# Performance work log

Measured on AMD Instinct MI355X. Metric: run time of the kernel, lower is better.

## Reference

```python
import jax, jax.numpy as jnp
import numpy as np

# Scaled Llama backbone (NF4 dequant-matmul == dense matmul math) + LoRA(q,v) + cls head
L, V, D, H, F, R, C = 4, 32000, 2048, 16, 8192, 16, 3
HD = D // H  # 128, matches real Llama head_dim
ALPHA_OVER_R = 32.0 / R
EPS = 1e-5
NEG = -1e9


def setup_inputs() -> dict:
    B, S = 2, 1024
    keys = iter(jax.random.split(jax.random.key(0), 40))

    def rn(shape, s=0.02):
        return jax.random.normal(next(keys), shape, dtype=jnp.float32) * s

    return {
        "input_ids": jax.random.randint(next(keys), (B, S), 0, V),
        "attention_mask": jnp.ones((B, S), dtype=jnp.int32),
        "embed": rn((V, D)),
        "Wq": rn((L, D, D)), "Wk": rn((L, D, D)), "Wv": rn((L, D, D)), "Wo": rn((L, D, D)),
        "Aq": rn((L, R, D)), "Bq": rn((L, D, R)), "Av": rn((L, R, D)), "Bv": rn((L, D, R)),
        "Wg": rn((L, F, D)), "Wu": rn((L, F, D)), "Wd": rn((L, D, F)),
        "norm1": jnp.ones((L, D)), "norm2": jnp.ones((L, D)), "final_norm": jnp.ones((D,)),
        "head_W1": rn((D, D)), "head_b1": jnp.zeros((D,)),
        "head_W2": rn((C, D)), "head_b2": jnp.zeros((C,)),
    }


def _rms(x, w):
    return x * w * jax.lax.rsqrt(jnp.mean(x * x, -1, keepdims=True) + EPS)


def _rope_tables(S):
    inv = 1.0 / (10000.0 ** (jnp.arange(0, HD, 2, dtype=jnp.float32) / HD))
    f = jnp.outer(jnp.arange(S, dtype=jnp.float32), inv)  # [S, HD//2]
    emb = jnp.concatenate([f, f], -1)                      # [S, HD]
    return jnp.cos(emb), jnp.sin(emb)


def _rot(x):
    return jnp.concatenate([-x[..., HD // 2:], x[..., :HD // 2]], -1)


def reference(input_ids, attention_mask, embed, Wq, Wk, Wv, Wo, Aq, Bq, Av, Bv,
              Wg, Wu, Wd, norm1, norm2, final_norm, head_W1, head_b1, head_W2, head_b2):
    B, S = input_ids.shape
    x = embed[input_ids]                                   # [B,S,D]
    cos, sin = _rope_tables(S)
    causal = jnp.tril(jnp.ones((S, S), dtype=bool))
    mask = jnp.where(causal[None, None], 0.0, NEG) \
        + (1.0 - attention_mask.astype(jnp.float32))[:, None, None, :] * NEG  # [B,1,S,S]

    for l in range(L):  # small fixed layer count
        h = _rms(x, norm1[l])

        def proj(W):
            return jnp.einsum('bsd,ed->bse', h, W)

        def lora(A, Bm):
            return ALPHA_OVER_R * jnp.einsum('bsr,er->bse', jnp.einsum('bsd,rd->bsr', h, A), Bm)

        q = (proj(Wq[l]) + lora(Aq[l], Bq[l])).reshape(B, S, H, HD)
        k = proj(Wk[l]).reshape(B, S, H, HD)
        v = (proj(Wv[l]) + lora(Av[l], Bv[l])).reshape(B, S, H, HD)
        q = q * cos[None, :, None, :] + _rot(q) * sin[None, :, None, :]
        k = k * cos[None, :, None, :] + _rot(k) * sin[None, :, None, :]

        scores = jnp.einsum('bqhd,bkhd->bhqk', q, k) / np.float32(np.sqrt(HD)) + mask
        attn = jax.nn.softmax(scores, -1)
        o = jnp.einsum('bhqk,bkhd->bqhd', attn, v).reshape(B, S, D)
        x = x + jnp.einsum('bsd,ed->bse', o, Wo[l])

        h2 = _rms(x, norm2[l])
        g = jnp.einsum('bsd,fd->bsf', h2, Wg[l])
        u = jnp.einsum('bsd,fd->bsf', h2, Wu[l])
        x = x + jnp.einsum('bsf,df->bsd', jax.nn.silu(g) * u, Wd[l])

    x = _rms(x, final_norm)
    # LlamaForSequenceClassification pooling at last non-pad token; score = Identity
    idx = jnp.sum(attention_mask, -1) - 1
    pooled = x[jnp.arange(B), idx].astype(jnp.float32)     # [B, D]
    # head_layer (dropout = identity in eval)
    h = jnp.tanh(pooled @ head_W1.T + head_b1)
    return h @ head_W2.T + head_b2                          # [B, C]
```

## Files before the change

kernel.cpp:

```cpp
#include <hip/hip_runtime.h>

#define NLAYER 4
#define DMODEL 2048
#define NHEAD  16
#define HEADD  128
#define FFDIM  8192
#define RLORA  16
#define SEQLEN 1024
#define NBATCH 2
#define NTOK   (NBATCH*SEQLEN)
#define QKVS   6144

typedef __bf16 bf16x8 __attribute__((ext_vector_type(8)));
typedef float  f32x4  __attribute__((ext_vector_type(4)));
typedef unsigned short us8 __attribute__((ext_vector_type(8)));

__device__ __forceinline__ unsigned short f2b(float f) {
  unsigned int u = __builtin_bit_cast(unsigned int, f);
  u += 0x7FFFu + ((u >> 16) & 1u);
  return (unsigned short)(u >> 16);
}
__device__ __forceinline__ float b2f(unsigned short s) {
  unsigned int u = ((unsigned int)s) << 16;
  return __builtin_bit_cast(float, u);
}
__device__ __forceinline__ int vswz(int d) {
  return (((d >> 2) & 7) ^ ((d & 3) << 1)) << 4;
}
typedef __attribute__((address_space(1))) const void* gas_t;
typedef __attribute__((address_space(3))) void* las_t;
__device__ __forceinline__ void gload16(const void* g, void* l) {
  __builtin_amdgcn_global_load_lds((gas_t)g, (las_t)l, 16, 0, 0);
}

__global__ void k_embed(const int* __restrict__ ids, const float* __restrict__ emb,
                        float* __restrict__ x) {
  int row = blockIdx.x;
  int id = ids[row];
  const float4* src = (const float4*)(emb + (size_t)id * DMODEL);
  float4* dst = (float4*)(x + (size_t)row * DMODEL);
  for (int i = threadIdx.x; i < DMODEL / 4; i += 256) dst[i] = src[i];
}

__global__ void k_cvt16(const float* __restrict__ s, unsigned short* __restrict__ d, int n8) {
  int stride = gridDim.x * 256;
  for (int i = blockIdx.x * 256 + threadIdx.x; i < n8; i += stride) {
    size_t si = (size_t)i * 2;
    float4 a = ((const float4*)s)[si];
    float4 b = ((const float4*)s)[si + 1];
    us8 o;
    o[0]=f2b(a.x); o[1]=f2b(a.y); o[2]=f2b(a.z); o[3]=f2b(a.w);
    o[4]=f2b(b.x); o[5]=f2b(b.y); o[6]=f2b(b.z); o[7]=f2b(b.w);
    ((us8*)d)[i] = o;
  }
}

__global__ void k_cvtqkv(const float* __restrict__ Wq, const float* __restrict__ Wk,
                         const float* __restrict__ Wv, unsigned short* __restrict__ d) {
  const size_t DD8 = (size_t)DMODEL * DMODEL / 8;
  const int n8 = (int)(NLAYER * 3 * DD8);
  int stride = gridDim.x * 256;
  for (int i = blockIdx.x * 256 + threadIdx.x; i < n8; i += stride) {
    int lay = i / (int)(3 * DD8);
    int rem = i - lay * (int)(3 * DD8);
    int ten = rem / (int)DD8;
    int off = rem - ten * (int)DD8;
    const float* s = (ten == 0 ? Wq : ten == 1 ? Wk : Wv) + (size_t)lay * DMODEL * DMODEL;
    float4 a = ((const float4*)s)[(size_t)off * 2];
    float4 b = ((const float4*)s)[(size_t)off * 2 + 1];
    us8 o;
    o[0]=f2b(a.x); o[1]=f2b(a.y); o[2]=f2b(a.z); o[3]=f2b(a.w);
    o[4]=f2b(b.x); o[5]=f2b(b.y); o[6]=f2b(b.z); o[7]=f2b(b.w);
    ((us8*)(d))[(size_t)i] = o;
  }
}

__global__ void k_rmsnorm(const float* __restrict__ x, const float* __restrict__ w,
                          unsigned short* __restrict__ h) {
  int row = blockIdx.x, t = threadIdx.x;
  const float* xr = x + (size_t)row * DMODEL;
  float4 a = ((const float4*)xr)[t];
  float4 b = ((const float4*)xr)[t + 256];
  float ss = a.x*a.x + a.y*a.y + a.z*a.z + a.w*a.w
           + b.x*b.x + b.y*b.y + b.z*b.z + b.w*b.w;
  for (int m = 32; m; m >>= 1) ss += __shfl_xor(ss, m);
  __shared__ float red[4];
  if ((t & 63) == 0) red[t >> 6] = ss;
  __syncthreads();
  ss = red[0] + red[1] + red[2] + red[3];
  float rs = rsqrtf(ss * (1.0f / DMODEL) + 1e-5f);
  float4 wa = ((const float4*)w)[t];
  float4 wb = ((const float4*)w)[t + 256];
  ushort4 oa, ob;
  oa.x = f2b(a.x * wa.x * rs); oa.y = f2b(a.y * wa.y * rs);
  oa.z = f2b(a.z * wa.z * rs); oa.w = f2b(a.w * wa.w * rs);
  ob.x = f2b(b.x * wb.x * rs); ob.y = f2b(b.y * wb.y * rs);
  ob.z = f2b(b.z * wb.z * rs); ob.w = f2b(b.w * wb.w * rs);
  ushort4* hr = (ushort4*)(h + (size_t)row * DMODEL);
  hr[t] = oa;
  hr[t + 256] = ob;
}

template<int MODE>
__global__ __launch_bounds__(512, 4)
void k_gemm5(const unsigned short* __restrict__ A, const unsigned short* __restrict__ B,
             float* __restrict__ Cf, unsigned short* __restrict__ Cb,
             const float* __restrict__ Res, const unsigned short* __restrict__ Gaux,
             int N, int K, int ldc) {
  __shared__ unsigned short As[8192];
  __shared__ unsigned short Bs[16384];
  const int t = threadIdx.x, l = t & 63, w = t >> 6;
  const int wm = w >> 2, wn = w & 3;
  const int nbx = gridDim.x;
  const int nwg = nbx * gridDim.y;
  const int bid = blockIdx.y * nbx + blockIdx.x;
  const int sid = (bid & 7) * (nwg >> 3) + (bid >> 3);
  const int m0 = (sid / nbx) << 7;
  const int n0 = (sid % nbx) << 8;
  const int srow = (w << 3) + (l >> 3);
  const int gcol = 8 * ((l & 7) ^ ((srow >> 1) & 7));
  const unsigned short* Ag = A + (size_t)(m0 + srow) * K + gcol;
  const unsigned short* Bg = B + (size_t)(n0 + srow) * K + gcol;
  const size_t r64K = (size_t)64 * K;
  unsigned short* AsW = As + (w << 9);
  unsigned short* BsW = Bs + (w << 9);
  const int cl = l & 15, lh = l >> 4;
  const int fR = (cl >> 1) & 7;
  f32x4 acc[4][4];
  #pragma unroll
  for (int mi = 0; mi < 4; mi++)
    #pragma unroll
    for (int ni = 0; ni < 4; ni++) { f32x4 z = {0.f,0.f,0.f,0.f}; acc[mi][ni] = z; }

  for (int kt = 0; kt < K; kt += 64) {
    gload16(Ag + kt,          AsW);
    gload16(Ag + kt +   r64K, AsW + 4096);
    gload16(Bg + kt,          BsW);
    gload16(Bg + kt +   r64K, BsW + 4096);
    gload16(Bg + kt + 2*r64K, BsW + 8192);
    gload16(Bg + kt + 3*r64K, BsW + 12288);
    __syncthreads();
    #pragma unroll
    for (int kh = 0; kh < 2; kh++) {
      const int so = ((kh * 4 + lh) ^ fR) << 4;
      bf16x8 af[4], bf[4];
      #pragma unroll
      for (int i = 0; i < 4; i++) {
        af[i] = *(const bf16x8*)((const char*)As + (wm*64 + i*16 + cl) * 128 + so);
        bf[i] = *(const bf16x8*)((const char*)Bs + (wn*64 + i*16 + cl) * 128 + so);
      }
      #pragma unroll
      for (int mi = 0; mi < 4; mi++)
        #pragma unroll
        for (int ni = 0; ni < 4; ni++)
          acc[mi][ni] = __builtin_amdgcn_mfma_f32_16x16x32_bf16(af[mi], bf[ni], acc[mi][ni], 0, 0, 0);
    }
    __syncthreads();
  }
  const int rbase = lh << 2;
  #pragma unroll
  for (int mi = 0; mi < 4; mi++) {
    #pragma unroll
    for (int ni = 0; ni < 4; ni++) {
      #pragma unroll
      for (int rr = 0; rr < 4; rr++) {
        int row = m0 + wm * 64 + mi * 16 + rbase + rr;
        int col = n0 + wn * 64 + ni * 16 + cl;
        size_t idx = (size_t)row * ldc + col;
        float val = acc[mi][ni][rr];
        if constexpr (MODE == 0) Cf[idx] = val;
        if constexpr (MODE == 1) Cf[idx] = val + Res[idx];
        if constexpr (MODE == 2) Cb[idx] = f2b(val);
        if constexpr (MODE == 3) {
          float gv = b2f(Gaux[idx]);
          val *= gv / (1.0f + __expf(-gv));
          Cb[idx] = f2b(val);
        }
      }
    }
  }
}

template<int MODE>
__global__ __launch_bounds__(256, 4)
void k_gemm6(const unsigned short* __restrict__ A, const unsigned short* __restrict__ B,
             float* __restrict__ Cf, unsigned short* __restrict__ Cb,
             const float* __restrict__ Res, const unsigned short* __restrict__ Gaux,
             int N, int K, int ldc) {
  __shared__ unsigned short As[4096];
  __shared__ unsigned short Bs[8192];
  const int t = threadIdx.x, l = t & 63, w = t >> 6;
  const int nbx = gridDim.x;
  const int nwg = nbx * gridDim.y;
  const int bid = blockIdx.y * nbx + blockIdx.x;
  const int sid = (bid & 7) * (nwg >> 3) + (bid >> 3);
  const int m0 = (sid / nbx) << 6;
  const int n0 = (sid % nbx) << 7;
  const int srow = (w << 3) + (l >> 3);
  const int gcol = 8 * ((l & 7) ^ ((srow >> 1) & 7));
  const unsigned short* Ag = A + (size_t)(m0 + srow) * K + gcol;
  const unsigned short* Bg = B + (size_t)(n0 + srow) * K + gcol;
  const size_t r32K = (size_t)32 * K;
  unsigned short* AsW = As + (w << 9);
  unsigned short* BsW = Bs + (w << 9);
  const int cl = l & 15, lh = l >> 4;
  const int fR = (cl >> 1) & 7;
  f32x4 acc[4][2];
  #pragma unroll
  for (int mi = 0; mi < 4; mi++)
    #pragma unroll
    for (int ni = 0; ni < 2; ni++) { f32x4 z = {0.f,0.f,0.f,0.f}; acc[mi][ni] = z; }

  for (int kt = 0; kt < K; kt += 64) {
    gload16(Ag + kt,          AsW);
    gload16(Ag + kt +   r32K, AsW + 2048);
    gload16(Bg + kt,          BsW);
    gload16(Bg + kt +   r32K, BsW + 2048);
    gload16(Bg + kt + 2*r32K, BsW + 4096);
    gload16(Bg + kt + 3*r32K, BsW + 6144);
    __syncthreads();
    #pragma unroll
    for (int kh = 0; kh < 2; kh++) {
      const int so = ((kh * 4 + lh) ^ fR) << 4;
      bf16x8 af[4], bf[2];
      #pragma unroll
      for (int mi = 0; mi < 4; mi++)
        af[mi] = *(const bf16x8*)((const char*)As + (mi*16 + cl) * 128 + so);
      #pragma unroll
      for (int ni = 0; ni < 2; ni++)
        bf[ni] = *(const bf16x8*)((const char*)Bs + (w*32 + ni*16 + cl) * 128 + so);
      #pragma unroll
      for (int mi = 0; mi < 4; mi++)
        #pragma unroll
        for (int ni = 0; ni < 2; ni++)
          acc[mi][ni] = __builtin_amdgcn_mfma_f32_16x16x32_bf16(af[mi], bf[ni], acc[mi][ni], 0, 0, 0);
    }
    __syncthreads();
  }
  const int rbase = lh << 2;
  #pragma unroll
  for (int mi = 0; mi < 4; mi++) {
    #pragma unroll
    for (int ni = 0; ni < 2; ni++) {
      #pragma unroll
      for (int rr = 0; rr < 4; rr++) {
        int row = m0 + mi * 16 + rbase + rr;
        int col = n0 + w * 32 + ni * 16 + cl;
        size_t idx = (size_t)row * ldc + col;
        float val = acc[mi][ni][rr];
        if constexpr (MODE == 0) Cf[idx] = val;
        if constexpr (MODE == 1) Cf[idx] = val + Res[idx];
        if constexpr (MODE == 2) Cb[idx] = f2b(val);
        if constexpr (MODE == 3) {
          float gv = b2f(Gaux[idx]);
          val *= gv / (1.0f + __expf(-gv));
          Cb[idx] = f2b(val);
        }
      }
    }
  }
}

template<int MODE>
__global__ __launch_bounds__(256, 2)
void k_gemm2(const unsigned short* __restrict__ A, const void* __restrict__ Bv,
             float* __restrict__ Cf, unsigned short* __restrict__ Cb,
             const float* __restrict__ Res, const unsigned short* __restrict__ Gaux,
             int N, int K, int ldc,
             const float* __restrict__ ltq, const float* __restrict__ ltv,
             const float* __restrict__ lbq, const float* __restrict__ lbv) {
  __shared__ unsigned short As[16384];
  __shared__ unsigned short Bs[16384];
  const unsigned short* B = (const unsigned short*)Bv;
  const int t = threadIdx.x, l = t & 63, w = t >> 6;
  const int wr = w >> 1, wc = w & 1;
  const int nbx = gridDim.x;
  const int nwg = nbx * gridDim.y;
  const int bid = blockIdx.y * nbx + blockIdx.x;
  const int sid = (bid & 7) * (nwg >> 3) + (bid >> 3);
  const int m0 = (sid / nbx) << 7, n0 = (sid % nbx) << 7;
  const int srow = (w << 3) + (l >> 3);
  const int gcol = 8 * ((l & 7) ^ ((srow >> 1) & 7));
  const unsigned short* Ag = A + (size_t)(m0 + srow) * K + gcol;
  const unsigned short* Bg = B + (size_t)(n0 + srow) * K + gcol;
  const size_t r32K = (size_t)32 * K;
  const int cl = l & 15, lh = l >> 4;
  const int fR = (cl >> 1) & 7;
  const int rowA = wr * 64 + cl;
  const int rowB = wc * 64 + cl;
  f32x4 acc[4][4];
  #pragma unroll
  for (int mi = 0; mi < 4; mi++)
    #pragma unroll
    for (int ni = 0; ni < 4; ni++) { f32x4 z = {0.f,0.f,0.f,0.f}; acc[mi][ni] = z; }

  const int NT = K >> 6;
#define STAGE2(buf, kt) do {                                        \
    const unsigned short* ap_ = Ag + (size_t)(kt) * 64;             \
    const unsigned short* bp_ = Bg + (size_t)(kt) * 64;             \
    unsigned short* al_ = As + (buf) * 8192 + (w << 9);             \
    unsigned short* bl_ = Bs + (buf) * 8192 + (w << 9);             \
    gload16(ap_,            al_);                                   \
    gload16(ap_ +   r32K,   al_ + 2048);                            \
    gload16(ap_ + 2*r32K,   al_ + 4096);                            \
    gload16(ap_ + 3*r32K,   al_ + 6144);                            \
    gload16(bp_,            bl_);                                   \
    gload16(bp_ +   r32K,   bl_ + 2048);                            \
    gload16(bp_ + 2*r32K,   bl_ + 4096);                            \
    gload16(bp_ + 3*r32K,   bl_ + 6144);                            \
  } while (0)

  STAGE2(0, 0);
  for (int kt = 0; kt < NT; kt++) {
    const int cur = kt & 1;
    if (kt + 1 < NT) {
      STAGE2(cur ^ 1, kt + 1);
      __builtin_amdgcn_sched_barrier(0);
      asm volatile("s_waitcnt vmcnt(8)" ::: "memory");
    } else {
      __builtin_amdgcn_sched_barrier(0);
      asm volatile("s_waitcnt vmcnt(0)" ::: "memory");
    }
    __builtin_amdgcn_s_barrier();
    __builtin_amdgcn_sched_barrier(0);
    const char* Ab = (const char*)As + cur * 16384;
    const char* Bb = (const char*)Bs + cur * 16384;
    #pragma unroll
    for (int kh = 0; kh < 2; kh++) {
      const int so = ((kh * 4 + lh) ^ fR) << 4;
      bf16x8 af[4], bf[4];
      #pragma unroll
      for (int i = 0; i < 4; i++) {
        af[i] = *(const bf16x8*)(Ab + (rowA + 16*i) * 128 + so);
        bf[i] = *(const bf16x8*)(Bb + (rowB + 16*i) * 128 + so);
      }
      #pragma unroll
      for (int mi = 0; mi < 4; mi++)
        #pragma unroll
        for (int ni = 0; ni < 4; ni++)
          acc[mi][ni] = __builtin_amdgcn_mfma_f32_16x16x32_bf16(af[mi], bf[ni], acc[mi][ni], 0, 0, 0);
    }
    __builtin_amdgcn_sched_barrier(0);
    __builtin_amdgcn_s_barrier();
  }
#undef STAGE2
  const int rbase = lh << 2;
  if constexpr (MODE == 4) {
    #pragma unroll
    for (int ni = 0; ni < 4; ni++) {
      int col = n0 + wc * 64 + ni * 16 + cl;
      const float* lt = nullptr;
      const float* lb = nullptr;
      if (col < 2048)       { lt = ltq; lb = lbq + (size_t)col * RLORA; }
      else if (col >= 4096) { lt = ltv; lb = lbv + (size_t)(col - 4096) * RLORA; }
      float4 b0 = {0,0,0,0}, b1 = b0, b2 = b0, b3 = b0;
      if (lt) {
        b0 = ((const float4*)lb)[0]; b1 = ((const float4*)lb)[1];
        b2 = ((const float4*)lb)[2]; b3 = ((const float4*)lb)[3];
      }
      #pragma unroll
      for (int mi = 0; mi < 4; mi++) {
        #pragma unroll
        for (int rr = 0; rr < 4; rr++) {
          int row = m0 + wr * 64 + mi * 16 + rbase + rr;
          float val = acc[mi][ni][rr];
          if (lt) {
            const float4* tr = (const float4*)(lt + (size_t)row * RLORA);
            float4 t0 = tr[0], t1 = tr[1], t2 = tr[2], t3 = tr[3];
            float dt = t0.x*b0.x + t0.y*b0.y + t0.z*b0.z + t0.w*b0.w
                     + t1.x*b1.x + t1.y*b1.y + t1.z*b1.z + t1.w*b1.w
                     + t2.x*b2.x + t2.y*b2.y + t2.z*b2.z + t2.w*b2.w
                     + t3.x*b3.x + t3.y*b3.y + t3.z*b3.z + t3.w*b3.w;
            val += 2.0f * dt;
          }
          Cf[(size_t)row * ldc + col] = val;
        }
      }
    }
  } else {
    #pragma unroll
    for (int mi = 0; mi < 4; mi++) {
      #pragma unroll
      for (int ni = 0; ni < 4; ni++) {
        #pragma unroll
        for (int rr = 0; rr < 4; rr++) {
          int row = m0 + wr * 64 + mi * 16 + rbase + rr;
          int col = n0 + wc * 64 + ni * 16 + cl;
          size_t idx = (size_t)row * ldc + col;
          float val = acc[mi][ni][rr];
          if constexpr (MODE == 0) Cf[idx] = val;
          if constexpr (MODE == 1) Cf[idx] = val + Res[idx];
          if constexpr (MODE == 2) Cb[idx] = f2b(val);
          if constexpr (MODE == 3) {
            float gv = b2f(Gaux[idx]);
            val *= gv / (1.0f + __expf(-gv));
            Cb[idx] = f2b(val);
          }
        }
      }
    }
  }
}

template<int MODE>
__global__ __launch_bounds__(256, 2)
void k_gemm(const unsigned short* __restrict__ A, const void* __restrict__ Bv,
            float* __restrict__ Cf, unsigned short* __restrict__ Cb,
            const float* __restrict__ Res, const unsigned short* __restrict__ Gaux,
            int N, int K, int ldc) {
  __shared__ unsigned char lds[128 * 32 * 2 * 2];
  unsigned char* As = lds;
  unsigned char* Bs = lds + 128 * 32 * 2;
  const int t = threadIdx.x;
  const int l = t & 63, w = t >> 6;
  const int wr = w >> 1, wc = w & 1;
  const int m0 = blockIdx.y << 7, n0 = blockIdx.x << 7;
  const int sr = t >> 1, skh = (t & 1) << 4;
  const int sByte = sr * 64 + (skh << 1);
  const int sSwz = (sr & 3) << 4;
  const unsigned short* Ap = A + (size_t)(m0 + sr) * K + skh;
  const float* Bp32 = (const float*)Bv + (size_t)(n0 + sr) * K + skh;
  const int kOff = (((l >> 4) << 4)) ^ ((l & 3) << 4);
  const int arow = wr * 64 + (l & 15);
  const int brow = wc * 64 + (l & 15);
  f32x4 acc[4][4];
  #pragma unroll
  for (int mi = 0; mi < 4; mi++)
    #pragma unroll
    for (int ni = 0; ni < 4; ni++) { f32x4 z = {0.f,0.f,0.f,0.f}; acc[mi][ni] = z; }

  for (int kt = 0; kt < K; kt += 32) {
    uint4 a0 = *(const uint4*)(Ap + kt);
    uint4 a1 = *(const uint4*)(Ap + kt + 8);
    *(uint4*)(As + ((sByte)      ^ sSwz)) = a0;
    *(uint4*)(As + ((sByte + 16) ^ sSwz)) = a1;
    float4 f0 = *(const float4*)(Bp32 + kt);
    float4 f1 = *(const float4*)(Bp32 + kt + 4);
    float4 f2 = *(const float4*)(Bp32 + kt + 8);
    float4 f3 = *(const float4*)(Bp32 + kt + 12);
    us8 q0, q1;
    q0[0]=f2b(f0.x); q0[1]=f2b(f0.y); q0[2]=f2b(f0.z); q0[3]=f2b(f0.w);
    q0[4]=f2b(f1.x); q0[5]=f2b(f1.y); q0[6]=f2b(f1.z); q0[7]=f2b(f1.w);
    q1[0]=f2b(f2.x); q1[1]=f2b(f2.y); q1[2]=f2b(f2.z); q1[3]=f2b(f2.w);
    q1[4]=f2b(f3.x); q1[5]=f2b(f3.y); q1[6]=f2b(f3.z); q1[7]=f2b(f3.w);
    *(us8*)(Bs + ((sByte)      ^ sSwz)) = q0;
    *(us8*)(Bs + ((sByte + 16) ^ sSwz)) = q1;
    __syncthreads();
    bf16x8 af[4], bfr[4];
    #pragma unroll
    for (int i = 0; i < 4; i++) {
      af[i]  = *(const bf16x8*)(As + (arow + 16 * i) * 64 + kOff);
      bfr[i] = *(const bf16x8*)(Bs + (brow + 16 * i) * 64 + kOff);
    }
    #pragma unroll
    for (int mi = 0; mi < 4; mi++)
      #pragma unroll
      for (int ni = 0; ni < 4; ni++)
        acc[mi][ni] = __builtin_amdgcn_mfma_f32_16x16x32_bf16(af[mi], bfr[ni], acc[mi][ni], 0, 0, 0);
    __syncthreads();
  }
  const int rbase = (l >> 4) << 2;
  const int cl = l & 15;
  #pragma unroll
  for (int mi = 0; mi < 4; mi++) {
    #pragma unroll
    for (int ni = 0; ni < 4; ni++) {
      #pragma unroll
      for (int rr = 0; rr < 4; rr++) {
        int row = m0 + wr * 64 + mi * 16 + rbase + rr;
        int col = n0 + wc * 64 + ni * 16 + cl;
        size_t idx = (size_t)row * ldc + col;
        float val = acc[mi][ni][rr];
        if constexpr (MODE == 0) Cf[idx] = val;
        if constexpr (MODE == 1) Cf[idx] = val + Res[idx];
        if constexpr (MODE == 2) Cb[idx] = f2b(val);
        if constexpr (MODE == 3) {
          float gv = b2f(Gaux[idx]);
          val *= gv / (1.0f + __expf(-gv));
          Cb[idx] = f2b(val);
        }
      }
    }
  }
}

__global__ void k_lora_down(const unsigned short* __restrict__ h, const float* __restrict__ Am,
                            float* __restrict__ tb) {
  int t = threadIdx.x;
  int m = blockIdx.x * 16 + (t >> 4), r = t & 15;
  const unsigned short* hr = h + (size_t)m * DMODEL;
  const float* ar = Am + (size_t)r * DMODEL;
  float acc = 0.f;
  for (int d = 0; d < DMODEL; d += 4) {
    ushort4 hv = *(const ushort4*)(hr + d);
    float4 av = *(const float4*)(ar + d);
    acc += b2f(hv.x)*av.x + b2f(hv.y)*av.y + b2f(hv.z)*av.z + b2f(hv.w)*av.w;
  }
  tb[(size_t)m * RLORA + r] = acc;
}

__global__ void k_lora_up(const float* __restrict__ tb, const float* __restrict__ Bm,
                          float* __restrict__ out, int ldc) {
  int tid = blockIdx.x * 256 + threadIdx.x;
  int m = tid >> 11, e = tid & (DMODEL - 1);
  const float* tr = tb + (size_t)m * RLORA;
  const float* br = Bm + (size_t)e * RLORA;
  float acc = 0.f;
  #pragma unroll
  for (int r = 0; r < RLORA; r += 4) {
    float4 tv = *(const float4*)(tr + r);
    float4 bv = *(const float4*)(br + r);
    acc += tv.x*bv.x + tv.y*bv.y + tv.z*bv.z + tv.w*bv.w;
  }
  out[(size_t)m * ldc + e] += 2.0f * acc;
}

__global__ void k_rope_table(float* __restrict__ ct, float* __restrict__ st) {
  int tid = blockIdx.x * 256 + threadIdx.x;
  int s = tid >> 6, i = tid & 63;
  float inv = __expf(-((float)i / 64.0f) * logf(10000.0f));
  float ang = (float)s * inv;
  ct[tid] = cosf(ang);
  st[tid] = sinf(ang);
}

__global__ void k_rope2(const float* __restrict__ qkv,
                        const float* __restrict__ ct, const float* __restrict__ st,
                        unsigned short* __restrict__ qb, unsigned short* __restrict__ kb,
                        unsigned short* __restrict__ vb) {
  int tid = blockIdx.x * 256 + threadIdx.x;
  int i = tid & 63;
  int hh = (tid >> 6) & (NHEAD - 1);
  int s = (tid >> 10) & (SEQLEN - 1);
  int b = tid >> 20;
  size_t ibase = ((size_t)(b * SEQLEN + s)) * QKVS + hh * HEADD;
  size_t obase = ((size_t)(b * SEQLEN + s)) * DMODEL + hh * HEADD;
  float c = ct[s * 64 + i], sn = st[s * 64 + i];
  float q0 = qkv[ibase + i], q1 = qkv[ibase + i + 64];
  qb[obase + i]      = f2b(q0 * c - q1 * sn);
  qb[obase + i + 64] = f2b(q1 * c + q0 * sn);
  float k0 = qkv[ibase + 2048 + i], k1 = qkv[ibase + 2048 + i + 64];
  kb[obase + i]      = f2b(k0 * c - k1 * sn);
  kb[obase + i + 64] = f2b(k1 * c + k0 * sn);
  vb[obase + i]      = f2b(qkv[ibase + 4096 + i]);
  vb[obase + i + 64] = f2b(qkv[ibase + 4096 + i + 64]);
}

__global__ __launch_bounds__(256, 2)
void k_attn_bf16(const unsigned short* __restrict__ qbp, const unsigned short* __restrict__ kbp,
                 const unsigned short* __restrict__ vbp, const int* __restrict__ am,
                 unsigned short* __restrict__ o, int vstride) {
  __shared__ unsigned char Kls[64 * 256];
  __shared__ unsigned char Vls[128 * 128];
  __shared__ unsigned char Pls[64 * 128];
  const int qt = blockIdx.x, hh = blockIdx.y, b = blockIdx.z;
  const int t = threadIdx.x, l = t & 63, w = t >> 6;
  const int cl = l & 15, lh = l >> 4;
  const int rbase = lh << 2;

  for (int ii = 0; ii < 4; ii++) {
    int idx = t + 256 * ii; int row = idx >> 4; int c = idx & 15;
    uint4 u = *(const uint4*)(qbp + ((size_t)(b*SEQLEN + qt*64 + row)) * DMODEL + hh * HEADD + c * 8);
    *(uint4*)(Kls + ((row * 256 + c * 16) ^ ((row & 7) << 4))) = u;
  }
  __syncthreads();
  bf16x8 qf[4];
  {
    int row = w * 16 + cl;
    int swz = (row & 7) << 4;
    #pragma unroll
    for (int kt = 0; kt < 4; kt++)
      qf[kt] = *(const bf16x8*)(Kls + ((row * 256 + kt * 64 + lh * 16) ^ swz));
  }

  f32x4 oacc[8];
  #pragma unroll
  for (int i = 0; i < 8; i++) { f32x4 z = {0.f,0.f,0.f,0.f}; oacc[i] = z; }
  float mrun[4], lrun[4];
  #pragma unroll
  for (int r = 0; r < 4; r++) { mrun[r] = -3e38f; lrun[r] = 0.f; }

  for (int kb = 0; kb <= qt; kb++) {
    __syncthreads();
    for (int ii = 0; ii < 4; ii++) {
      int idx = t + 256 * ii; int row = idx >> 4; int c = idx & 15;
      uint4 u = *(const uint4*)(kbp + ((size_t)(b*SEQLEN + kb*64 + row)) * DMODEL + hh * HEADD + c * 8);
      *(uint4*)(Kls + ((row * 256 + c * 16) ^ ((row & 7) << 4))) = u;
    }
    for (int ii = 0; ii < 4; ii++) {
      int idx = t + 256 * ii;
      int n = idx >> 4, dc = idx & 15;
      uint4 a = *(const uint4*)(vbp + ((size_t)(b*SEQLEN + kb*64 + n)) * vstride + hh * HEADD + dc * 8);
      uint4 p;
      p.x = __shfl_xor(a.x, 16); p.y = __shfl_xor(a.y, 16);
      p.z = __shfl_xor(a.z, 16); p.w = __shfl_xor(a.w, 16);
      if (!(l & 16)) {
        int d0 = dc * 8, nb = n * 2;
        unsigned int wd[8];
        wd[0] = (a.x & 0xffffu) | (p.x << 16);
        wd[1] = (a.x >> 16)     | (p.x & 0xffff0000u);
        wd[2] = (a.y & 0xffffu) | (p.y << 16);
        wd[3] = (a.y >> 16)     | (p.y & 0xffff0000u);
        wd[4] = (a.z & 0xffffu) | (p.z << 16);
        wd[5] = (a.z >> 16)     | (p.z & 0xffff0000u);
        wd[6] = (a.w & 0xffffu) | (p.w << 16);
        wd[7] = (a.w >> 16)     | (p.w & 0xffff0000u);
        #pragma unroll
        for (int e = 0; e < 8; e++)
          *(unsigned int*)(Vls + (((d0 + e) * 128 + nb) ^ vswz(d0 + e))) = wd[e];
      }
    }
    __syncthreads();
    f32x4 sacc[4];
    #pragma unroll
    for (int nt = 0; nt < 4; nt++) { f32x4 z = {0.f,0.f,0.f,0.f}; sacc[nt] = z; }
    #pragma unroll
    for (int kt = 0; kt < 4; kt++) {
      #pragma unroll
      for (int nt = 0; nt < 4; nt++) {
        int row = nt * 16 + cl;
        bf16x8 kf = *(const bf16x8*)(Kls + ((row * 256 + kt * 64 + lh * 16) ^ ((row & 7) << 4)));
        sacc[nt] = __builtin_amdgcn_mfma_f32_16x16x32_bf16(qf[kt], kf, sacc[nt], 0, 0, 0);
      }
    }
    float p[4][4];
    float mt[4] = {-3e38f, -3e38f, -3e38f, -3e38f};
    #pragma unroll
    for (int nt = 0; nt < 4; nt++) {
      int kg = kb * 64 + nt * 16 + cl;
      float pad = (1.0f - (float)am[b * SEQLEN + kg]) * (-1e9f);
      #pragma unroll
      for (int r = 0; r < 4; r++) {
        int qg = qt * 64 + w * 16 + rbase + r;
        float s = sacc[nt][r] * 0.08838834764831845f + pad;
        if (kg > qg) s = -1e30f;
        p[nt][r] = s;
        mt[r] = fmaxf(mt[r], s);
      }
    }
    #pragma unroll
    for (int r = 0; r < 4; r++) {
      float m = mt[r];
      m = fmaxf(m, __shfl_xor(m, 1)); m = fmaxf(m, __shfl_xor(m, 2));
      m = fmaxf(m, __shfl_xor(m, 4)); m = fmaxf(m, __shfl_xor(m, 8));
      mt[r] = m;
    }
    float corr[4];
    #pragma unroll
    for (int r = 0; r < 4; r++) {
      float mnew = fmaxf(mrun[r], mt[r]);
      corr[r] = __expf(mrun[r] - mnew);
      mrun[r] = mnew;
    }
    float ps[4] = {0.f, 0.f, 0.f, 0.f};
    #pragma unroll
    for (int nt = 0; nt < 4; nt++)
      #pragma unroll
      for (int r = 0; r < 4; r++) {
        p[nt][r] = __expf(p[nt][r] - mrun[r]);
        ps[r] += p[nt][r];
      }
    #pragma unroll
    for (int r = 0; r < 4; r++) {
      float s = ps[r];
      s += __shfl_xor(s, 1); s += __shfl_xor(s, 2);
      s += __shfl_xor(s, 4); s += __shfl_xor(s, 8);
      lrun[r] = lrun[r] * corr[r] + s;
    }
    #pragma unroll
    for (int nt = 0; nt < 4; nt++)
      #pragma unroll
      for (int r = 0; r < 4; r++) {
        int row = w * 16 + rbase + r;
        *(unsigned short*)(Pls + ((row * 128 + (nt * 16 + cl) * 2) ^ ((row & 7) << 4))) = f2b(p[nt][r]);
      }
    #pragma unroll
    for (int dt = 0; dt < 8; dt++)
      #pragma unroll
      for (int r = 0; r < 4; r++) oacc[dt][r] *= corr[r];
    {
      int prow = w * 16 + cl, pswz = (prow & 7) << 4;
      bf16x8 pf0 = *(const bf16x8*)(Pls + ((prow * 128 +  0 + lh * 16) ^ pswz));
      bf16x8 pf1 = *(const bf16x8*)(Pls + ((prow * 128 + 64 + lh * 16) ^ pswz));
      #pragma unroll
      for (int dt = 0; dt < 8; dt++) {
        int drow = dt * 16 + cl;
        bf16x8 vf0 = *(const bf16x8*)(Vls + ((drow * 128 +  0 + lh * 16) ^ vswz(drow)));
        bf16x8 vf1 = *(const bf16x8*)(Vls + ((drow * 128 + 64 + lh * 16) ^ vswz(drow)));
        oacc[dt] = __builtin_amdgcn_mfma_f32_16x16x32_bf16(pf0, vf0, oacc[dt], 0, 0, 0);
        oacc[dt] = __builtin_amdgcn_mfma_f32_16x16x32_bf16(pf1, vf1, oacc[dt], 0, 0, 0);
      }
    }
  }
  size_t obase = (((size_t)b * SEQLEN + qt * 64 + w * 16) * NHEAD + hh) * HEADD;
  #pragma unroll
  for (int r = 0; r < 4; r++) {
    float inv = 1.0f / lrun[r];
    int row = rbase + r;
    #pragma unroll
    for (int dt = 0; dt < 8; dt++)
      o[obase + (size_t)row * (NHEAD * HEADD) + dt * 16 + cl] = f2b(oacc[dt][r] * inv);
  }
}

__global__ void k_pool(const float* __restrict__ x, const int* __restrict__ am,
                       const float* __restrict__ fn, float* __restrict__ pooled) {
  int b = blockIdx.x, t = threadIdx.x;
  __shared__ float red[4];
  float fc = 0.f;
  for (int i = t; i < SEQLEN; i += 256) fc += (float)am[b * SEQLEN + i];
  for (int m = 32; m; m >>= 1) fc += __shfl_xor(fc, m);
  if ((t & 63) == 0) red[t >> 6] = fc;
  __syncthreads();
  int idx = (int)(red[0] + red[1] + red[2] + red[3]) - 1;
  const float* xr = x + ((size_t)b * SEQLEN + idx) * DMODEL;
  float4 a = ((const float4*)xr)[t], c = ((const float4*)xr)[t + 256];
  float ss = a.x*a.x + a.y*a.y + a.z*a.z + a.w*a.w
           + c.x*c.x + c.y*c.y + c.z*c.z + c.w*c.w;
  for (int m = 32; m; m >>= 1) ss += __shfl_xor(ss, m);
  __syncthreads();
  if ((t & 63) == 0) red[t >> 6] = ss;
  __syncthreads();
  ss = red[0] + red[1] + red[2] + red[3];
  float rs = rsqrtf(ss * (1.0f / DMODEL) + 1e-5f);
  float4 w0 = ((const float4*)fn)[t], w1 = ((const float4*)fn)[t + 256];
  float4 o0, o1;
  o0.x = a.x*rs*w0.x; o0.y = a.y*rs*w0.y; o0.z = a.z*rs*w0.z; o0.w = a.w*rs*w0.w;
  o1.x = c.x*rs*w1.x; o1.y = c.y*rs*w1.y; o1.z = c.z*rs*w1.z; o1.w = c.w*rs*w1.w;
  ((float4*)(pooled + (size_t)b * DMODEL))[t] = o0;
  ((float4*)(pooled + (size_t)b * DMODEL))[t + 256] = o1;
}

__global__ void k_head1(const float* __restrict__ pooled, const float* __restrict__ W1,
                        const float* __restrict__ b1, float* __restrict__ h1) {
  int bi = blockIdx.x;
  int b = bi >> 3, e = ((bi & 7) << 8) + threadIdx.x;
  const float* pr = pooled + (size_t)b * DMODEL;
  const float* wr = W1 + (size_t)e * DMODEL;
  float acc = 0.f;
  for (int d = 0; d < DMODEL; d += 4) {
    float4 pv = *(const float4*)(pr + d);
    float4 wv = *(const float4*)(wr + d);
    acc += pv.x*wv.x + pv.y*wv.y + pv.z*wv.z + pv.w*wv.w;
  }
  h1[(size_t)b * DMODEL + e] = tanhf(acc + b1[e]);
}

__global__ void k_head2(const float* __restrict__ h1, const float* __restrict__ W2,
                        const float* __restrict__ b2, float* __restrict__ out) {
  int bi = blockIdx.x;
  int b = bi / 3, c = bi % 3;
  int l = threadIdx.x;
  float acc = 0.f;
  for (int e = l; e < DMODEL; e += 64)
    acc += h1[(size_t)b * DMODEL + e] * W2[(size_t)c * DMODEL + e];
  for (int m = 32; m; m >>= 1) acc += __shfl_xor(acc, m);
  if (l == 0) out[b * 3 + c] = acc + b2[c];
}

__global__ void k_sentinel(float* out) {
  if (threadIdx.x < 6) out[threadIdx.x] = -12345.0f;
}

extern "C" void kernel_launch(void* const* d_in, const int* in_sizes, int n_in,
                              void* d_out, int out_size, void* d_ws, size_t ws_size,
                              hipStream_t stream) {
  const int*   ids = (const int*)d_in[0];
  const int*   am  = (const int*)d_in[1];
  const float* emb = (const float*)d_in[2];
  const float* Wq  = (const float*)d_in[3];
  const float* Wk  = (const float*)d_in[4];
  const float* Wv  = (const float*)d_in[5];
  const float* Wo  = (const float*)d_in[6];
  const float* Aq  = (const float*)d_in[7];
  const float* Bq  = (const float*)d_in[8];
  const float* Av  = (const float*)d_in[9];
  const float* Bv  = (const float*)d_in[10];
  const float* Wg  = (const float*)d_in[11];
  const float* Wu  = (const float*)d_in[12];
  const float* Wd  = (const float*)d_in[13];
  const float* n1  = (const float*)d_in[14];
  const float* n2  = (const float*)d_in[15];
  const float* fn  = (const float*)d_in[16];
  const float* hW1 = (const float*)d_in[17];
  const float* hb1 = (const float*)d_in[18];
  const float* hW2 = (const float*)d_in[19];
  const float* hb2 = (const float*)d_in[20];
  float* out = (float*)d_out;

  const size_t XOFF    = 0;
  const size_t HOFF    = 16777216;
  const size_t QBOFF   = 25165824;
  const size_t KBOFF   = 33554432;
  const size_t VBOFF   = 41943040;
  const size_t OOFF    = 50331648;
  const size_t GOFF    = 58720256;
  const size_t ACTOFF  = 92274688;
  const size_t QKV32OFF= 125829120;
  const size_t TOFF    = 176160768;
  const size_t NEED = TOFF + 131072 + 131072 + 262144 + 262144 + 16384 + 16384;
  if (ws_size < NEED) {
    k_sentinel<<<1, 64, 0, stream>>>(out);
    return;
  }
  const size_t W16OFF   = (NEED + 255) & ~(size_t)255;
  const size_t W16BYTES = 536870912ull;
  const bool   use16    = ws_size >= W16OFF + W16BYTES;

  char* ws = (char*)d_ws;
  float*          x     = (float*)(ws + XOFF);
  unsigned short* h     = (unsigned short*)(ws + HOFF);
  unsigned short* qb    = (unsigned short*)(ws + QBOFF);
  unsigned short* kb    = (unsigned short*)(ws + KBOFF);
  unsigned short* vb    = (unsigned short*)(ws + VBOFF);
  unsigned short* o     = (unsigned short*)(ws + OOFF);
  unsigned short* g     = (unsigned short*)(ws + GOFF);
  unsigned short* act   = (unsigned short*)(ws + ACTOFF);
  float*          qkv32 = (float*)(ws + QKV32OFF);
  float* tbq    = (float*)(ws + TOFF);
  float* tbv    = (float*)(ws + TOFF + 131072);
  float* ct     = (float*)(ws + TOFF + 262144);
  float* st     = (float*)(ws + TOFF + 262144 + 262144);
  float* pooled = (float*)(ws + TOFF + 262144 + 524288);
  float* h1     = (float*)(ws + TOFF + 262144 + 524288 + 16384);

  unsigned short* w16 = (unsigned short*)(ws + W16OFF);
  const size_t DD = (size_t)DMODEL * DMODEL;
  const size_t FD = (size_t)FFDIM * DMODEL;
  unsigned short* wqkv16 = w16;
  unsigned short* wo16   = w16 + 4ull * 3 * DD;
  unsigned short* wg16   = wo16 + 4ull * DD;
  unsigned short* wu16   = wg16 + 4ull * FD;
  unsigned short* wd16   = wu16 + 4ull * FD;
  if (use16) {
    k_cvtqkv<<<2048, 256, 0, stream>>>(Wq, Wk, Wv, wqkv16);
    k_cvt16<<<2048, 256, 0, stream>>>(Wo, wo16, (int)(4 * DD / 8));
    k_cvt16<<<2048, 256, 0, stream>>>(Wg, wg16, (int)(4 * FD / 8));
    k_cvt16<<<2048, 256, 0, stream>>>(Wu, wu16, (int)(4 * FD / 8));
    k_cvt16<<<2048, 256, 0, stream>>>(Wd, wd16, (int)(4 * FD / 8));
  }

  k_embed<<<NTOK, 256, 0, stream>>>(ids, emb, x);
  k_rope_table<<<SEQLEN * 64 / 256, 256, 0, stream>>>(ct, st);

  dim3 g16(16, 16), gqkv(48, 16), gffn(32, 16), gsq(16, 32), ga(SEQLEN / 64, NHEAD, NBATCH);
  for (int lay = 0; lay < NLAYER; lay++) {
    const float* Bq_l = Bq + (size_t)lay * DMODEL * RLORA;
    const float* Bv_l = Bv + (size_t)lay * DMODEL * RLORA;
    k_rmsnorm<<<NTOK, 256, 0, stream>>>(x, n1 + (size_t)lay * DMODEL, h);
    k_lora_down<<<NTOK / 16, 256, 0, stream>>>(h, Aq + (size_t)lay * RLORA * DMODEL, tbq);
    k_lora_down<<<NTOK / 16, 256, 0, stream>>>(h, Av + (size_t)lay * RLORA * DMODEL, tbv);
    if (use16) {
      k_gemm2<4><<<gqkv, 256, 0, stream>>>(h, wqkv16 + lay*3*DD, qkv32, nullptr, nullptr, nullptr,
                                           QKVS, DMODEL, QKVS, tbq, tbv, Bq_l, Bv_l);
      k_rope2<<<NBATCH * SEQLEN * NHEAD * 64 / 256, 256, 0, stream>>>(qkv32, ct, st, qb, kb, vb);
      k_attn_bf16<<<ga, 256, 0, stream>>>(qb, kb, vb, am, o, DMODEL);
      k_gemm6<1><<<gsq, 256, 0, stream>>>(o, wo16 + lay*DD, x, nullptr, x, nullptr, DMODEL, DMODEL, DMODEL);
      k_rmsnorm<<<NTOK, 256, 0, stream>>>(x, n2 + (size_t)lay * DMODEL, h);
      k_gemm5<2><<<gffn, 512, 0, stream>>>(h, wg16 + lay*FD, nullptr, g, nullptr, nullptr, FFDIM, DMODEL, FFDIM);
      k_gemm5<3><<<gffn, 512, 0, stream>>>(h, wu16 + lay*FD, nullptr, act, nullptr, g, FFDIM, DMODEL, FFDIM);
      k_gemm6<1><<<gsq, 256, 0, stream>>>(act, wd16 + lay*FD, x, nullptr, x, nullptr, DMODEL, FFDIM, DMODEL);
    } else {
      k_gemm<0><<<g16, 256, 0, stream>>>(h, Wq + lay*DD, qkv32,        nullptr, nullptr, nullptr, DMODEL, DMODEL, QKVS);
      k_gemm<0><<<g16, 256, 0, stream>>>(h, Wk + lay*DD, qkv32 + 2048, nullptr, nullptr, nullptr, DMODEL, DMODEL, QKVS);
      k_gemm<0><<<g16, 256, 0, stream>>>(h, Wv + lay*DD, qkv32 + 4096, nullptr, nullptr, nullptr, DMODEL, DMODEL, QKVS);
      k_lora_up<<<NTOK * DMODEL / 256, 256, 0, stream>>>(tbq, Bq_l, qkv32, QKVS);
      k_lora_up<<<NTOK * DMODEL / 256, 256, 0, stream>>>(tbv, Bv_l, qkv32 + 4096, QKVS);
      k_rope2<<<NBATCH * SEQLEN * NHEAD * 64 / 256, 256, 0, stream>>>(qkv32, ct, st, qb, kb, vb);
      k_attn_bf16<<<ga, 256, 0, stream>>>(qb, kb, vb, am, o, DMODEL);
      k_gemm<1><<<g16, 256, 0, stream>>>(o, Wo + lay*DD, x, nullptr, x, nullptr, DMODEL, DMODEL, DMODEL);
      k_rmsnorm<<<NTOK, 256, 0, stream>>>(x, n2 + (size_t)lay * DMODEL, h);
      k_gemm<2><<<dim3(64,16), 256, 0, stream>>>(h, Wg + lay*FD, nullptr, g, nullptr, nullptr, FFDIM, DMODEL, FFDIM);
      k_gemm<3><<<dim3(64,16), 256, 0, stream>>>(h, Wu + lay*FD, nullptr, act, nullptr, g, FFDIM, DMODEL, FFDIM);
      k_gemm<1><<<g16, 256, 0, stream>>>(act, Wd + lay*FD, x, nullptr, x, nullptr, DMODEL, FFDIM, DMODEL);
    }
  }
  k_pool<<<NBATCH, 256, 0, stream>>>(x, am, fn, pooled);
  k_head1<<<16, 256, 0, stream>>>(pooled, hW1, hb1, h1);
  k_head2<<<6, 64, 0, stream>>>(h1, hW2, hb2, out);
}
```

Baseline: 3.093 ms.

## Fuse gate and up projections into one SwiGLU GEMM kernel, retile QKV GEMM

Replaces the two separate gate and up GEMMs with one kernel that loads the activation tile once, accumulates both projections, and applies SiLU(g)*u in the epilogue. This removes the bf16 round trip of the gate tensor through global memory and halves A-tile loads for the FFN. The QKV GEMM is replaced by a smaller 64x128 tile, single-buffered kernel with more blocks and higher occupancy, dropping the previous double-buffered pipeline. The weight-convert index math also switches from divides to shifts.

New measurement: 3.083 ms. About the same (-0.3%).

```diff
diff --git a/kernel.cpp b/kernel.cpp
--- a/kernel.cpp
+++ b/kernel.cpp
@@ -61,10 +61,10 @@
   const int n8 = (int)(NLAYER * 3 * DD8);
   int stride = gridDim.x * 256;
   for (int i = blockIdx.x * 256 + threadIdx.x; i < n8; i += stride) {
-    int lay = i / (int)(3 * DD8);
-    int rem = i - lay * (int)(3 * DD8);
-    int ten = rem / (int)DD8;
-    int off = rem - ten * (int)DD8;
+    int blk = i >> 19;
+    int lay = blk / 3;
+    int ten = blk - lay * 3;
+    int off = i & ((1 << 19) - 1);
     const float* s = (ten == 0 ? Wq : ten == 1 ? Wk : Wv) + (size_t)lay * DMODEL * DMODEL;
     float4 a = ((const float4*)s)[(size_t)off * 2];
     float4 b = ((const float4*)s)[(size_t)off * 2 + 1];
@@ -101,14 +101,13 @@
   hr[t + 256] = ob;
 }
 
-template<int MODE>
 __global__ __launch_bounds__(512, 4)
-void k_gemm5(const unsigned short* __restrict__ A, const unsigned short* __restrict__ B,
-             float* __restrict__ Cf, unsigned short* __restrict__ Cb,
-             const float* __restrict__ Res, const unsigned short* __restrict__ Gaux,
-             int N, int K, int ldc) {
+void k_ffn(const unsigned short* __restrict__ A, const unsigned short* __restrict__ Bgw,
+           const unsigned short* __restrict__ Buw, unsigned short* __restrict__ act,
+           int N, int K, int ldc) {
   __shared__ unsigned short As[8192];
-  __shared__ unsigned short Bs[16384];
+  __shared__ unsigned short Gs[8192];
+  __shared__ unsigned short Us[8192];
   const int t = threadIdx.x, l = t & 63, w = t >> 6;
   const int wm = w >> 2, wn = w & 3;
   const int nbx = gridDim.x;
@@ -116,44 +115,54 @@
   const int bid = blockIdx.y * nbx + blockIdx.x;
   const int sid = (bid & 7) * (nwg >> 3) + (bid >> 3);
   const int m0 = (sid / nbx) << 7;
-  const int n0 = (sid % nbx) << 8;
+  const int n0 = (sid % nbx) << 7;
   const int srow = (w << 3) + (l >> 3);
   const int gcol = 8 * ((l & 7) ^ ((srow >> 1) & 7));
-  const unsigned short* Ag = A + (size_t)(m0 + srow) * K + gcol;
-  const unsigned short* Bg = B + (size_t)(n0 + srow) * K + gcol;
+  const unsigned short* Ap = A   + (size_t)(m0 + srow) * K + gcol;
+  const unsigned short* Gp = Bgw + (size_t)(n0 + srow) * K + gcol;
+  const unsigned short* Up = Buw + (size_t)(n0 + srow) * K + gcol;
   const size_t r64K = (size_t)64 * K;
   unsigned short* AsW = As + (w << 9);
-  unsigned short* BsW = Bs + (w << 9);
+  unsigned short* GsW = Gs + (w << 9);
+  unsigned short* UsW = Us + (w << 9);
   const int cl = l & 15, lh = l >> 4;
   const int fR = (cl >> 1) & 7;
-  f32x4 acc[4][4];
+  f32x4 ag[4][2], au[4][2];
   #pragma unroll
   for (int mi = 0; mi < 4; mi++)
     #pragma unroll
-    for (int ni = 0; ni < 4; ni++) { f32x4 z = {0.f,0.f,0.f,0.f}; acc[mi][ni] = z; }
+    for (int ni = 0; ni < 2; ni++) {
+      f32x4 z = {0.f,0.f,0.f,0.f};
+      ag[mi][ni] = z; au[mi][ni] = z;
+    }
 
   for (int kt = 0; kt < K; kt += 64) {
-    gload16(Ag + kt,          AsW);
-    gload16(Ag + kt +   r64K, AsW + 4096);
-    gload16(Bg + kt,          BsW);
-    gload16(Bg + kt +   r64K, BsW + 4096);
-    gload16(Bg + kt + 2*r64K, BsW + 8192);
-    gload16(Bg + kt + 3*r64K, BsW + 12288);
+    gload16(Ap + kt,          AsW);
+    gload16(Ap + kt + r64K,   AsW + 4096);
+    gload16(Gp + kt,          GsW);
+    gload16(Gp + kt + r64K,   GsW + 4096);
+    gload16(Up + kt,          UsW);
+    gload16(Up + kt + r64K,   UsW + 4096);
     __syncthreads();
     #pragma unroll
     for (int kh = 0; kh < 2; kh++) {
       const int so = ((kh * 4 + lh) ^ fR) << 4;
-      bf16x8 af[4], bf[4];
-      #pragma unroll
-      for (int i = 0; i < 4; i++) {
-        af[i] = *(const bf16x8*)((const char*)As + (wm*64 + i*16 + cl) * 128 + so);
-        bf[i] = *(const bf16x8*)((const char*)Bs + (wn*64 + i*16 + cl) * 128 + so);
+      bf16x8 af[4], bg[2], bu[2];
+      #pragma unroll
+      for (int mi = 0; mi < 4; mi++)
+        af[mi] = *(const bf16x8*)((const char*)As + (wm*64 + mi*16 + cl) * 128 + so);
+      #pragma unroll
+      for (int ni = 0; ni < 2; ni++) {
+        bg[ni] = *(const bf16x8*)((const char*)Gs + (wn*32 + ni*16 + cl) * 128 + so);
+        bu[ni] = *(const bf16x8*)((const char*)Us + (wn*32 + ni*16 + cl) * 128 + so);
       }
       #pragma unroll
       for (int mi = 0; mi < 4; mi++)
         #pragma unroll
-        for (int ni = 0; ni < 4; ni++)
-          acc[mi][ni] = __builtin_amdgcn_mfma_f32_16x16x32_bf16(af[mi], bf[ni], acc[mi][ni], 0, 0, 0);
+        for (int ni = 0; ni < 2; ni++) {
+          ag[mi][ni] = __builtin_amdgcn_mfma_f32_16x16x32_bf16(af[mi], bg[ni], ag[mi][ni], 0, 0, 0);
+          au[mi][ni] = __builtin_amdgcn_mfma_f32_16x16x32_bf16(af[mi], bu[ni], au[mi][ni], 0, 0, 0);
+        }
     }
     __syncthreads();
   }
@@ -161,21 +170,15 @@
   #pragma unroll
   for (int mi = 0; mi < 4; mi++) {
     #pragma unroll
-    for (int ni = 0; ni < 4; ni++) {
+    for (int ni = 0; ni < 2; ni++) {
       #pragma unroll
       for (int rr = 0; rr < 4; rr++) {
         int row = m0 + wm * 64 + mi * 16 + rbase + rr;
-        int col = n0 + wn * 64 + ni * 16 + cl;
-        size_t idx = (size_t)row * ldc + col;
-        float val = acc[mi][ni][rr];
-        if constexpr (MODE == 0) Cf[idx] = val;
-        if constexpr (MODE == 1) Cf[idx] = val + Res[idx];
-        if constexpr (MODE == 2) Cb[idx] = f2b(val);
-        if constexpr (MODE == 3) {
-          float gv = b2f(Gaux[idx]);
-          val *= gv / (1.0f + __expf(-gv));
-          Cb[idx] = f2b(val);
-        }
+        int col = n0 + wn * 32 + ni * 16 + cl;
+        float gv = ag[mi][ni][rr];
+        float uv = au[mi][ni][rr];
+        float val = gv / (1.0f + __expf(-gv)) * uv;
+        act[(size_t)row * ldc + col] = f2b(val);
       }
     }
   }
@@ -261,142 +264,90 @@
   }
 }
 
-template<int MODE>
-__global__ __launch_bounds__(256, 2)
-void k_gemm2(const unsigned short* __restrict__ A, const void* __restrict__ Bv,
-             float* __restrict__ Cf, unsigned short* __restrict__ Cb,
-             const float* __restrict__ Res, const unsigned short* __restrict__ Gaux,
-             int N, int K, int ldc,
+__global__ __launch_bounds__(256, 4)
+void k_gemm7(const unsigned short* __restrict__ A, const unsigned short* __restrict__ B,
+             float* __restrict__ Cf, int N, int K, int ldc,
              const float* __restrict__ ltq, const float* __restrict__ ltv,
              const float* __restrict__ lbq, const float* __restrict__ lbv) {
-  __shared__ unsigned short As[16384];
-  __shared__ unsigned short Bs[16384];
-  const unsigned short* B = (const unsigned short*)Bv;
+  __shared__ unsigned short As[4096];
+  __shared__ unsigned short Bs[8192];
   const int t = threadIdx.x, l = t & 63, w = t >> 6;
-  const int wr = w >> 1, wc = w & 1;
   const int nbx = gridDim.x;
   const int nwg = nbx * gridDim.y;
   const int bid = blockIdx.y * nbx + blockIdx.x;
   const int sid = (bid & 7) * (nwg >> 3) + (bid >> 3);
-  const int m0 = (sid / nbx) << 7, n0 = (sid % nbx) << 7;
+  const int m0 = (sid / nbx) << 6;
+  const int n0 = (sid % nbx) << 7;
   const int srow = (w << 3) + (l >> 3);
   const int gcol = 8 * ((l & 7) ^ ((srow >> 1) & 7));
   const unsigned short* Ag = A + (size_t)(m0 + srow) * K + gcol;
   const unsigned short* Bg = B + (size_t)(n0 + srow) * K + gcol;
   const size_t r32K = (size_t)32 * K;
+  unsigned short* AsW = As + (w << 9);
+  unsigned short* BsW = Bs + (w << 9);
   const int cl = l & 15, lh = l >> 4;
   const int fR = (cl >> 1) & 7;
-  const int rowA = wr * 64 + cl;
-  const int rowB = wc * 64 + cl;
-  f32x4 acc[4][4];
+  f32x4 acc[4][2];
   #pragma unroll
   for (int mi = 0; mi < 4; mi++)
     #pragma unroll
-    for (int ni = 0; ni < 4; ni++) { f32x4 z = {0.f,0.f,0.f,0.f}; acc[mi][ni] = z; }
-
-  const int NT = K >> 6;
-#define STAGE2(buf, kt) do {                                        \
-    const unsigned short* ap_ = Ag + (size_t)(kt) * 64;             \
-    const unsigned short* bp_ = Bg + (size_t)(kt) * 64;             \
-    unsigned short* al_ = As + (buf) * 8192 + (w << 9);             \
-    unsigned short* bl_ = Bs + (buf) * 8192 + (w << 9);             \
-    gload16(ap_,            al_);                                   \
-    gload16(ap_ +   r32K,   al_ + 2048);                            \
-    gload16(ap_ + 2*r32K,   al_ + 4096);                            \
-    gload16(ap_ + 3*r32K,   al_ + 6144);                            \
-    gload16(bp_,            bl_);                                   \
-    gload16(bp_ +   r32K,   bl_ + 2048);                            \
-    gload16(bp_ + 2*r32K,   bl_ + 4096);                            \
-    gload16(bp_ + 3*r32K,   bl_ + 6144);                            \
-  } while (0)
-
-  STAGE2(0, 0);
-  for (int kt = 0; kt < NT; kt++) {
-    const int cur = kt & 1;
-    if (kt + 1 < NT) {
-      STAGE2(cur ^ 1, kt + 1);
-      __builtin_amdgcn_sched_barrier(0);
-      asm volatile("s_waitcnt vmcnt(8)" ::: "memory");
-    } else {
-      __builtin_amdgcn_sched_barrier(0);
-      asm volatile("s_waitcnt vmcnt(0)" ::: "memory");
-    }
-    __builtin_amdgcn_s_barrier();
-    __builtin_amdgcn_sched_barrier(0);
-    const char* Ab = (const char*)As + cur * 16384;
-    const char* Bb = (const char*)Bs + cur * 16384;
+    for (int ni = 0; ni < 2; ni++) { f32x4 z = {0.f,0.f,0.f,0.f}; acc[mi][ni] = z; }
+
+  for (int kt = 0; kt < K; kt += 64) {
+    gload16(Ag + kt,          AsW);
+    gload16(Ag + kt +   r32K, AsW + 2048);
+    gload16(Bg + kt,          BsW);
+    gload16(Bg + kt +   r32K, BsW + 2048);
+    gload16(Bg + kt + 2*r32K, BsW + 4096);
+    gload16(Bg + kt + 3*r32K, BsW + 6144);
+    __syncthreads();
     #pragma unroll
     for (int kh = 0; kh < 2; kh++) {
       const int so = ((kh * 4 + lh) ^ fR) << 4;
-      bf16x8 af[4], bf[4];
-      #pragma unroll
-      for (int i = 0; i < 4; i++) {
-        af[i] = *(const bf16x8*)(Ab + (rowA + 16*i) * 128 + so);
-        bf[i] = *(const bf16x8*)(Bb + (rowB + 16*i) * 128 + so);
-      }
+      bf16x8 af[4], bf[2];
+      #pragma unroll
+      for (int mi = 0; mi < 4; mi++)
+        af[mi] = *(const bf16x8*)((const char*)As + (mi*16 + cl) * 128 + so);
+      #pragma unroll
+      for (int ni = 0; ni < 2; ni++)
+        bf[ni] = *(const bf16x8*)((const char*)Bs + (w*32 + ni*16 + cl) * 128 + so);
       #pragma unroll
       for (int mi = 0; mi < 4; mi++)
         #pragma unroll
-        for (int ni = 0; ni < 4; ni++)
+        for (int ni = 0; ni < 2; ni++)
           acc[mi][ni] = __builtin_amdgcn_mfma_f32_16x16x32_bf16(af[mi], bf[ni], acc[mi][ni], 0, 0, 0);
     }
-    __builtin_amdgcn_sched_barrier(0);
-    __builtin_amdgcn_s_barrier();
-  }
-#undef STAGE2
+    __syncthreads();
+  }
   const int rbase = lh << 2;
-  if constexpr (MODE == 4) {
-    #pragma unroll
-    for (int ni = 0; ni < 4; ni++) {
-      int col = n0 + wc * 64 + ni * 16 + cl;
-      const float* lt = nullptr;
-      const float* lb = nullptr;
-      if (col < 2048)       { lt = ltq; lb = lbq + (size_t)col * RLORA; }
-      else if (col >= 4096) { lt = ltv; lb = lbv + (size_t)(col - 4096) * RLORA; }
-      float4 b0 = {0,0,0,0}, b1 = b0, b2 = b0, b3 = b0;
-      if (lt) {
-        b0 = ((const float4*)lb)[0]; b1 = ((const float4*)lb)[1];
-        b2 = ((const float4*)lb)[2]; b3 = ((const float4*)lb)[3];
-      }
-      #pragma unroll
-      for (int mi = 0; mi < 4; mi++) {
-        #pragma unroll
-        for (int rr = 0; rr < 4; rr++) {
-          int row = m0 + wr * 64 + mi * 16 + rbase + rr;
-          float val = acc[mi][ni][rr];
-          if (lt) {
-            const float4* tr = (const float4*)(lt + (size_t)row * RLORA);
-            float4 t0 = tr[0], t1 = tr[1], t2 = tr[2], t3 = tr[3];
-            float dt = t0.x*b0.x + t0.y*b0.y + t0.z*b0.z + t0.w*b0.w
-                     + t1.x*b1.x + t1.y*b1.y + t1.z*b1.z + t1.w*b1.w
-                     + t2.x*b2.x + t2.y*b2.y + t2.z*b2.z + t2.w*b2.w
-                     + t3.x*b3.x + t3.y*b3.y + t3.z*b3.z + t3.w*b3.w;
-            val += 2.0f * dt;
-          }
-          Cf[(size_t)row * ldc + col] = val;
+  #pragma unroll
+  for (int ni = 0; ni < 2; ni++) {
+    int col = n0 + w * 32 + ni * 16 + cl;
+    const float* lt = nullptr;
+    const float* lb = nullptr;
+    if (col < 2048)       { lt = ltq; lb = lbq + (size_t)col * RLORA; }
+    else if (col >= 4096) { lt = ltv; lb = lbv + (size_t)(col - 4096) * RLORA; }
+    float4 b0 = {0,0,0,0}, b1 = b0, b2 = b0, b3 = b0;
+    if (lt) {
+      b0 = ((const float4*)lb)[0]; b1 = ((const float4*)lb)[1];
+      b2 = ((const float4*)lb)[2]; b3 = ((const float4*)lb)[3];
+    }
+    #pragma unroll
+    for (int mi = 0; mi < 4; mi++) {
+      #pragma unroll
+      for (int rr = 0; rr < 4; rr++) {
+        int row = m0 + mi * 16 + rbase + rr;
+        float val = acc[mi][ni][rr];
+        if (lt) {
+          const float4* tr = (const float4*)(lt + (size_t)row * RLORA);
+          float4 t0 = tr[0], t1 = tr[1], t2 = tr[2], t3 = tr[3];
+          float dt = t0.x*b0.x + t0.y*b0.y + t0.z*b0.z + t0.w*b0.w
+                   + t1.x*b1.x + t1.y*b1.y + t1.z*b1.z + t1.w*b1.w
+                   + t2.x*b2.x + t2.y*b2.y + t2.z*b2.z + t2.w*b2.w
+                   + t3.x*b3.x + t3.y*b3.y + t3.z*b3.z + t3.w*b3.w;
+          val += 2.0f * dt;
         }
-      }
-    }
-  } else {
-    #pragma unroll
-    for (int mi = 0; mi < 4; mi++) {
-      #pragma unroll
-      for (int ni = 0; ni < 4; ni++) {
-        #pragma unroll
-        for (int rr = 0; rr < 4; rr++) {
-          int row = m0 + wr * 64 + mi * 16 + rbase + rr;
-          int col = n0 + wc * 64 + ni * 16 + cl;
-          size_t idx = (size_t)row * ldc + col;
-          float val = acc[mi][ni][rr];
-          if constexpr (MODE == 0) Cf[idx] = val;
-          if constexpr (MODE == 1) Cf[idx] = val + Res[idx];
-          if constexpr (MODE == 2) Cb[idx] = f2b(val);
-          if constexpr (MODE == 3) {
-            float gv = b2f(Gaux[idx]);
-            val *= gv / (1.0f + __expf(-gv));
-            Cb[idx] = f2b(val);
-          }
-        }
+        Cf[(size_t)row * ldc + col] = val;
       }
     }
   }
@@ -843,7 +794,7 @@
   k_embed<<<NTOK, 256, 0, stream>>>(ids, emb, x);
   k_rope_table<<<SEQLEN * 64 / 256, 256, 0, stream>>>(ct, st);
 
-  dim3 g16(16, 16), gqkv(48, 16), gffn(32, 16), gsq(16, 32), ga(SEQLEN / 64, NHEAD, NBATCH);
+  dim3 g16(16, 16), gqkv(48, 32), gffn(64, 16), gsq(16, 32), ga(SEQLEN / 64, NHEAD, NBATCH);
   for (int lay = 0; lay < NLAYER; lay++) {
     const float* Bq_l = Bq + (size_t)lay * DMODEL * RLORA;
     const float* Bv_l = Bv + (size_t)lay * DMODEL * RLORA;
@@ -851,14 +802,13 @@
     k_lora_down<<<NTOK / 16, 256, 0, stream>>>(h, Aq + (size_t)lay * RLORA * DMODEL, tbq);
     k_lora_down<<<NTOK / 16, 256, 0, stream>>>(h, Av + (size_t)lay * RLORA * DMODEL, tbv);
     if (use16) {
-      k_gemm2<4><<<gqkv, 256, 0, stream>>>(h, wqkv16 + lay*3*DD, qkv32, nullptr, nullptr, nullptr,
-                                           QKVS, DMODEL, QKVS, tbq, tbv, Bq_l, Bv_l);
+      k_gemm7<<<gqkv, 256, 0, stream>>>(h, wqkv16 + lay*3*DD, qkv32,
+                                        QKVS, DMODEL, QKVS, tbq, tbv, Bq_l, Bv_l);
       k_rope2<<<NBATCH * SEQLEN * NHEAD * 64 / 256, 256, 0, stream>>>(qkv32, ct, st, qb, kb, vb);
       k_attn_bf16<<<ga, 256, 0, stream>>>(qb, kb, vb, am, o, DMODEL);
       k_gemm6<1><<<gsq, 256, 0, stream>>>(o, wo16 + lay*DD, x, nullptr, x, nullptr, DMODEL, DMODEL, DMODEL);
       k_rmsnorm<<<NTOK, 256, 0, stream>>>(x, n2 + (size_t)lay * DMODEL, h);
-      k_gemm5<2><<<gffn, 512, 0, stream>>>(h, wg16 + lay*FD, nullptr, g, nullptr, nullptr, FFDIM, DMODEL, FFDIM);
-      k_gemm5<3><<<gffn, 512, 0, stream>>>(h, wu16 + lay*FD, nullptr, act, nullptr, g, FFDIM, DMODEL, FFDIM);
+      k_ffn<<<gffn, 512, 0, stream>>>(h, wg16 + lay*FD, wu16 + lay*FD, act, FFDIM, DMODEL, FFDIM);
       k_gemm6<1><<<gsq, 256, 0, stream>>>(act, wd16 + lay*FD, x, nullptr, x, nullptr, DMODEL, FFDIM, DMODEL);
     } else {
       k_gemm<0><<<g16, 256, 0, stream>>>(h, Wq + lay*DD, qkv32,        nullptr, nullptr, nullptr, DMODEL, DMODEL, QKVS);
```
